# Performance work log

Measured on AMD Instinct MI355X. Metric: run time of the kernel, lower is better.

Reference implementation:

```python
import jax, jax.numpy as jnp
import numpy as np

B, N, C = 64, 256, 1024
H = 16
D = C // H            # head_dim = 64
HALF = D // 2         # rope dim per axis = 32
PT = 16               # hw_seq_len
THETA = 10000.0


def build_rope_tables():
    # VisionRotaryEmbeddingFast: per-axis freqs, repeated r=2, 2D broadcat
    freqs = 1.0 / (THETA ** (np.arange(0, HALF, 2, dtype=np.float32) / HALF))  # [HALF/2]=16
    t = np.arange(PT, dtype=np.float32)                                        # ft==pt -> t=arange
    f = t[:, None] * freqs[None, :]                                            # [16,16]
    f = np.repeat(f, 2, axis=-1)                                               # [16,32]
    f2d = np.concatenate(
        [np.broadcast_to(f[:, None, :], (PT, PT, HALF)),
         np.broadcast_to(f[None, :, :], (PT, PT, HALF))], axis=-1)             # [16,16,64]
    f2d = f2d.reshape(PT * PT, D)                                              # [256,64]
    return jnp.asarray(np.cos(f2d)), jnp.asarray(np.sin(f2d))


def rotate_half(t):
    # (..., d) -> pairwise (x0,x1) -> (-x1, x0)
    t2 = t.reshape(*t.shape[:-1], -1, 2)
    return jnp.stack([-t2[..., 1], t2[..., 0]], axis=-1).reshape(t.shape)


def apply_rope(t, cos, sin):
    # t: [B,H,N,D]; cos/sin: [N,D]
    return t * cos + rotate_half(t) * sin


def setup_inputs() -> dict:
    key = jax.random.key(0)
    k1, k2, k3 = jax.random.split(key, 3)
    x = jax.random.normal(k1, (B, N, C), dtype=jnp.float32)
    mask = jnp.ones((1, 1, N, N), dtype=bool)  # True = attend (SDPA bool mask)
    qkv_w = jax.random.normal(k2, (3 * C, C), dtype=jnp.float32) * 0.02
    qkv_b = jnp.zeros((3 * C,), dtype=jnp.float32)
    proj_w = jax.random.normal(k3, (C, C), dtype=jnp.float32) * 0.02
    proj_b = jnp.zeros((C,), dtype=jnp.float32)
    rope_cos, rope_sin = build_rope_tables()
    return {"x": x, "mask": mask, "qkv_w": qkv_w, "qkv_b": qkv_b,
            "proj_w": proj_w, "proj_b": proj_b,
            "rope_cos": rope_cos, "rope_sin": rope_sin}


def reference(x, mask, qkv_w, qkv_b, proj_w, proj_b, rope_cos, rope_sin):
    b, n, c = x.shape
    scale = 1.0 / jnp.sqrt(jnp.asarray(D, x.dtype))
    qkv = x @ qkv_w.T + qkv_b                              # [B,N,3C]
    qkv = qkv.reshape(b, n, 3, H, D).transpose(2, 0, 3, 1, 4)  # [3,B,H,N,D]
    q, k, v = qkv[0], qkv[1], qkv[2]
    q = apply_rope(q, rope_cos, rope_sin)
    k = apply_rope(k, rope_cos, rope_sin)
    scores = jnp.einsum('bhnd,bhmd->bhnm', q, k) * scale   # [B,H,N,N]
    neg = jnp.asarray(jnp.finfo(scores.dtype).min, scores.dtype)
    scores = jnp.where(mask, scores, neg)
    attn = jax.nn.softmax(scores, axis=-1)
    out = jnp.einsum('bhnm,bhmd->bhnd', attn, v)           # [B,H,N,D]
    out = out.transpose(0, 2, 1, 3).reshape(b, n, c)       # [B,N,C]
    return out @ proj_w.T + proj_b
```

## Files before the change

### kernel.cpp

```cpp
#include <hip/hip_runtime.h>
#include <math.h>

typedef short s16x8 __attribute__((ext_vector_type(8)));
typedef float f32x4 __attribute__((ext_vector_type(4)));

#define DEV static __device__ __forceinline__

DEV unsigned short f2bf(float f){
  unsigned int u = __builtin_bit_cast(unsigned int, f);
  u += 0x7fffu + ((u >> 16) & 1u);
  return (unsigned short)(u >> 16);
}

DEV void gload_lds16(const void* g, void* l){
  __builtin_amdgcn_global_load_lds(
      (const __attribute__((address_space(1))) unsigned int*)g,
      (__attribute__((address_space(3))) unsigned int*)l,
      16, 0, 0);
}

__global__ void cvt_bf16(const float* __restrict__ in, short* __restrict__ out, int n8){
  int i = blockIdx.x*blockDim.x + threadIdx.x;
  if (i >= n8) return;
  const float* p = in + (size_t)i*8;
  f32x4 a = *(const f32x4*)(p);
  f32x4 b = *(const f32x4*)(p+4);
  s16x8 o;
#pragma unroll
  for (int j=0;j<4;++j){ o[j] = (short)f2bf(a[j]); o[4+j] = (short)f2bf(b[j]); }
  *(s16x8*)(out + (size_t)i*8) = o;
}

template<int EPI>
DEV void stage_half(const short* __restrict__ Ag, const short* __restrict__ Bg,
                    char* buf, int m0, int n0, int k0, int wid, int lane, int half){
  const int l8 = lane >> 3, l7 = lane & 7;
  const int cole = ((l7 ^ l8) << 3) + k0;
#pragma unroll
  for (int j = 0; j < 2; ++j){
    const int chunk = (half*2 + j)*8 + wid;
    const short* src = Ag + (size_t)(m0 + chunk*8 + l8)*1024 + cole;
    gload_lds16(src, buf + chunk*1024);
  }
  {
    const int chunk = half*8 + wid;
    const short* src = Bg + (size_t)(n0 + chunk*8 + l8)*1024 + cole;
    gload_lds16(src, buf + 32768 + chunk*1024);
  }
}

template<int EPI>
__global__ __launch_bounds__(512, 2)
void gemm_dp(const short* __restrict__ A, const short* __restrict__ Bw,
             const float* __restrict__ bias,
             const float* __restrict__ cosT, const float* __restrict__ sinT,
             short* __restrict__ q_out, short* __restrict__ k_out, short* __restrict__ v_out,
             float* __restrict__ f_out)
{
  constexpr int K  = 1024;
  constexpr int BK = 64;
  constexpr int NT = K / BK;
  constexpr int NX = (EPI == 0) ? 24 : 8;
  constexpr int TB = 49152;
  __shared__ char smem[3 * TB];

  const int tid  = threadIdx.x;
  const int lane = tid & 63;
  const int wid  = tid >> 6;
  const int wm   = wid >> 2;
  const int wn   = wid & 3;
  const int lr   = lane & 15;
  const int lk   = lane >> 4;

  const int nwg = NX * 64;
  const int bid = blockIdx.x;
  const int cpx = nwg >> 3;
  const int swz = (bid & 7) * cpx + (bid >> 3);
  const int mt  = swz / NX;
  int nt        = swz % NX;
  if (mt & 1) nt = NX - 1 - nt;
  const int m0  = mt * 256;
  const int n0  = nt * 128;

  char* b0 = smem;
  char* b1 = smem + TB;
  char* b2 = smem + 2*TB;

  stage_half<EPI>(A, Bw, b0, m0, n0, 0,  wid, lane, 0);
  stage_half<EPI>(A, Bw, b0, m0, n0, 0,  wid, lane, 1);
  stage_half<EPI>(A, Bw, b1, m0, n0, BK, wid, lane, 0);
  stage_half<EPI>(A, Bw, b1, m0, n0, BK, wid, lane, 1);
  asm volatile("s_waitcnt vmcnt(6)" ::: "memory");
  asm volatile("s_barrier" ::: "memory");

  f32x4 acc[8][2] = {};

  for (int t = 0; t < NT; ++t){
    const int ks = (t + 2 < NT ? (t + 2) : (NT - 1)) * BK;
#pragma unroll
    for (int kk = 0; kk < 2; ++kk){
      s16x8 af[8], bf[2];
      const int cb = kk*64 + lk*16;
#pragma unroll
      for (int m = 0; m < 8; ++m){
        const int row = wm*128 + m*16 + lr;
        af[m] = *(const s16x8*)(b0 + row*128 + (cb ^ ((row & 7) << 4)));
      }
#pragma unroll
      for (int n = 0; n < 2; ++n){
        const int row = wn*32 + n*16 + lr;
        bf[n] = *(const s16x8*)(b0 + 32768 + row*128 + (cb ^ ((row & 7) << 4)));
      }
      stage_half<EPI>(A, Bw, b2, m0, n0, ks, wid, lane, kk);
      asm volatile("s_barrier" ::: "memory");
      __builtin_amdgcn_s_setprio(1);
#pragma unroll
      for (int m = 0; m < 8; ++m)
#pragma unroll
        for (int n = 0; n < 2; ++n)
          acc[m][n] = __builtin_amdgcn_mfma_f32_16x16x32_bf16(af[m], bf[n], acc[m][n], 0, 0, 0);
      __builtin_amdgcn_s_setprio(0);
    }
    asm volatile("s_waitcnt vmcnt(6)" ::: "memory");
    asm volatile("s_barrier" ::: "memory");
    char* tmp = b0; b0 = b1; b1 = b2; b2 = tmp;
  }
  asm volatile("s_waitcnt vmcnt(0)" ::: "memory");

  if constexpr (EPI == 0){
    const int sel = n0 >> 10;
    short* dst0 = (sel == 0) ? q_out : k_out;
#pragma unroll
    for (int m = 0; m < 8; ++m){
#pragma unroll
      for (int n = 0; n < 2; ++n){
        const int col  = n0 + wn*32 + n*16 + lr;
        const int rowb = m0 + wm*128 + m*16 + lk*4;
        const float bv = bias[col];
        const int rem = col & 1023;
        const int h = rem >> 6, d = rem & 63;
        if (sel < 2){
#pragma unroll
          for (int r = 0; r < 4; ++r){
            const int row = rowb + r;
            const int ntok = row & 255, b = row >> 8;
            float v = acc[m][n][r] + bv;
            float partner = __shfl_xor(v, 1, 64);
            float rot = (lane & 1) ? partner : -partner;
            float o = v * cosT[ntok*64 + d] + rot * sinT[ntok*64 + d];
            if (sel == 0) o *= 0.125f;
            dst0[(((size_t)b*16 + h)*256 + ntok)*64 + d] = (short)f2bf(o);
          }
        } else {
          const int ntok = rowb & 255, b = rowb >> 8;
          unsigned long long pk = 0;
#pragma unroll
          for (int r = 0; r < 4; ++r)
            pk |= ((unsigned long long)f2bf(acc[m][n][r] + bv)) << (16*r);
          *(unsigned long long*)(v_out + (((size_t)b*16 + h)*64 + d)*256 + ntok) = pk;
        }
      }
    }
  } else {
#pragma unroll
    for (int m = 0; m < 8; ++m){
#pragma unroll
      for (int n = 0; n < 2; ++n){
        const int col  = n0 + wn*32 + n*16 + lr;
        const int rowb = m0 + wm*128 + m*16 + lk*4;
        const float bv = bias[col];
#pragma unroll
        for (int r = 0; r < 4; ++r)
          f_out[(size_t)(rowb + r)*1024 + col] = acc[m][n][r] + bv;
      }
    }
  }
}

__global__ __launch_bounds__(512)
void attn_kernel(const short* __restrict__ qh, const short* __restrict__ kh,
                 const short* __restrict__ vt, short* __restrict__ ao)
{
  __shared__ short Ks[256*64];
  __shared__ short Vs[64*256];
  __shared__ short Ps[8][32*64];
  const int tid  = threadIdx.x;
  const int lane = tid & 63;
  const int wid  = tid >> 6;
  const int lr   = lane & 15;
  const int lk   = lane >> 4;
  const int bh = blockIdx.x;
  const size_t base = (size_t)bh * 256 * 64;
  const short* Kg = kh + base;
  const short* Qg = qh + base;
  const short* Vg = vt + base;

#pragma unroll
  for (int p=0; p<4; ++p){
    int flat = (p*512 + tid)*8;
    uint4 kv = *(const uint4*)(Kg + flat);
    int krow = flat >> 6;  int kcb = (flat & 63)*2;
    *(uint4*)((char*)Ks + krow*128 + (kcb ^ ((krow&7)<<4))) = kv;
    uint4 vv = *(const uint4*)(Vg + flat);
    int vrow = flat >> 8;  int vcb = (flat & 255)*2;
    *(uint4*)((char*)Vs + vrow*512 + (vcb ^ ((vrow&7)<<4))) = vv;
  }

  const int qbase = wid*32;
  s16x8 qf[2][2];
#pragma unroll
  for (int qr=0; qr<2; ++qr)
#pragma unroll
    for (int ks=0; ks<2; ++ks)
      qf[qr][ks] = *(const s16x8*)(Qg + (size_t)(qbase + qr*16 + lr)*64 + ks*32 + lk*8);

  __syncthreads();

  float mrun[2][4], lrun[2][4];
  f32x4 o[2][4] = {};
#pragma unroll
  for (int qr=0; qr<2; ++qr)
#pragma unroll
    for (int r=0; r<4; ++r){ mrun[qr][r] = -INFINITY; lrun[qr][r] = 0.f; }

  for (int t=0; t<4; ++t){
    f32x4 s[2][4] = {};
#pragma unroll
    for (int kc=0; kc<4; ++kc){
      const int row = t*64 + kc*16 + lr;
#pragma unroll
      for (int ks=0; ks<2; ++ks){
        const int cb = ks*64 + lk*16;
        s16x8 kf = *(const s16x8*)((char*)Ks + row*128 + (cb ^ ((row&7)<<4)));
#pragma unroll
        for (int qr=0; qr<2; ++qr)
          s[qr][kc] = __builtin_amdgcn_mfma_f32_16x16x32_bf16(qf[qr][ks], kf, s[qr][kc], 0, 0, 0);
      }
    }
#pragma unroll
    for (int qr=0; qr<2; ++qr)
#pragma unroll
      for (int r=0; r<4; ++r){
        float mx = fmaxf(fmaxf(s[qr][0][r], s[qr][1][r]), fmaxf(s[qr][2][r], s[qr][3][r]));
        mx = fmaxf(mx, __shfl_xor(mx, 1, 64));
        mx = fmaxf(mx, __shfl_xor(mx, 2, 64));
        mx = fmaxf(mx, __shfl_xor(mx, 4, 64));
        mx = fmaxf(mx, __shfl_xor(mx, 8, 64));
        const float mnew  = fmaxf(mrun[qr][r], mx);
        const float alpha = __expf(mrun[qr][r] - mnew);
        float rsum = 0.f;
#pragma unroll
        for (int kc=0; kc<4; ++kc){
          float p = __expf(s[qr][kc][r] - mnew);
          s[qr][kc][r] = p;
          rsum += p;
        }
        rsum += __shfl_xor(rsum, 1, 64);
        rsum += __shfl_xor(rsum, 2, 64);
        rsum += __shfl_xor(rsum, 4, 64);
        rsum += __shfl_xor(rsum, 8, 64);
        lrun[qr][r] = lrun[qr][r]*alpha + rsum;
        mrun[qr][r] = mnew;
#pragma unroll
        for (int oc=0; oc<4; ++oc) o[qr][oc][r] *= alpha;
      }
#pragma unroll
    for (int qr=0; qr<2; ++qr)
#pragma unroll
      for (int kc=0; kc<4; ++kc)
#pragma unroll
        for (int r=0; r<4; ++r){
          const int row = qr*16 + lk*4 + r;
          const int cb  = (kc*16 + lr)*2;
          *(short*)((char*)&Ps[wid][0] + row*128 + (cb ^ ((row&7)<<4))) = (short)f2bf(s[qr][kc][r]);
        }
#pragma unroll
    for (int ks2=0; ks2<2; ++ks2){
      s16x8 pf[2];
#pragma unroll
      for (int qr=0; qr<2; ++qr){
        const int row = qr*16 + lr;
        const int cb  = ks2*64 + lk*16;
        pf[qr] = *(const s16x8*)((char*)&Ps[wid][0] + row*128 + (cb ^ ((row&7)<<4)));
      }
#pragma unroll
      for (int oc=0; oc<4; ++oc){
        const int vrow = oc*16 + lr;
        const int vcb  = t*128 + ks2*64 + lk*16;
        s16x8 vf = *(const s16x8*)((char*)Vs + vrow*512 + (vcb ^ ((vrow&7)<<4)));
#pragma unroll
        for (int qr=0; qr<2; ++qr)
          o[qr][oc] = __builtin_amdgcn_mfma_f32_16x16x32_bf16(pf[qr], vf, o[qr][oc], 0, 0, 0);
      }
    }
  }

  const int b = bh >> 4, h = bh & 15;
#pragma unroll
  for (int qr=0; qr<2; ++qr)
#pragma unroll
    for (int oc=0; oc<4; ++oc)
#pragma unroll
      for (int r=0; r<4; ++r){
        const int n = qbase + qr*16 + lk*4 + r;
        const int d = oc*16 + lr;
        float val = o[qr][oc][r] / lrun[qr][r];
        ao[(size_t)(b*256 + n)*1024 + h*64 + d] = (short)f2bf(val);
      }
}

extern "C" void kernel_launch(void* const* d_in, const int* in_sizes, int n_in,
                              void* d_out, int out_size, void* d_ws, size_t ws_size,
                              hipStream_t stream)
{
  const float* x      = (const float*)d_in[0];
  const float* qkv_w  = (const float*)d_in[2];
  const float* qkv_b  = (const float*)d_in[3];
  const float* proj_w = (const float*)d_in[4];
  const float* proj_b = (const float*)d_in[5];
  const float* rc     = (const float*)d_in[6];
  const float* rs     = (const float*)d_in[7];

  char* ws = (char*)d_ws;
  short* xbf   = (short*)(ws);
  short* wqkv  = (short*)(ws + 33554432);
  short* wproj = (short*)(ws + 39845888);
  short* qhb   = (short*)(ws + 41943040);
  short* khb   = (short*)(ws + 75497472);
  short* vtb   = (short*)(ws + 109051904);
  short* aob   = xbf;

  cvt_bf16<<<8192, 256, 0, stream>>>(x,      xbf,   2097152);
  cvt_bf16<<<1536, 256, 0, stream>>>(qkv_w,  wqkv,   393216);
  cvt_bf16<<< 512, 256, 0, stream>>>(proj_w, wproj,  131072);

  gemm_dp<0><<<1536, 512, 0, stream>>>(xbf, wqkv, qkv_b, rc, rs,
                                       qhb, khb, vtb, nullptr);
  attn_kernel<<<1024, 512, 0, stream>>>(qhb, khb, vtb, aob);
  gemm_dp<1><<<512, 512, 0, stream>>>(aob, wproj, proj_b, nullptr, nullptr,
                                      nullptr, nullptr, nullptr, (float*)d_out);
}
```

Before: 386.9 us.

## Enlarge GEMM tiles to 256x256, double-buffer LDS, fuse bf16 conversions into one launch

The GEMM tile grows from 256x128 to 256x256, with each wave computing 8x4 MFMA blocks, which raises arithmetic intensity per staged byte. The triple-buffered half-stage pipeline with mid-iteration barriers becomes a simpler double buffer that waits for all loads at the end of each k-step. The three fp32-to-bf16 conversion launches merge into one kernel that picks its source by index range. In exchange, accumulator registers double (risking spills under launch_bounds(512,2)), LDS use is 128KB, grids shrink to 768 and 256 blocks, which may underfill the 256 CUs, and less load latency is hidden.

```diff
diff --git a/kernel.cpp b/kernel.cpp
--- a/kernel.cpp
+++ b/kernel.cpp
@@ -19,50 +19,54 @@
       16, 0, 0);
 }
 
-__global__ void cvt_bf16(const float* __restrict__ in, short* __restrict__ out, int n8){
+__global__ void cvt_all(const float* __restrict__ x,  const float* __restrict__ w1,
+                        const float* __restrict__ w2,
+                        short* __restrict__ ox, short* __restrict__ o1,
+                        short* __restrict__ o2){
   int i = blockIdx.x*blockDim.x + threadIdx.x;
-  if (i >= n8) return;
-  const float* p = in + (size_t)i*8;
+  const float* src; short* dst; int j;
+  if (i < 2097152)      { src = x;  dst = ox; j = i; }
+  else if (i < 2490368) { src = w1; dst = o1; j = i - 2097152; }
+  else                  { src = w2; dst = o2; j = i - 2490368; }
+  const float* p = src + (size_t)j*8;
   f32x4 a = *(const f32x4*)(p);
   f32x4 b = *(const f32x4*)(p+4);
   s16x8 o;
 #pragma unroll
-  for (int j=0;j<4;++j){ o[j] = (short)f2bf(a[j]); o[4+j] = (short)f2bf(b[j]); }
-  *(s16x8*)(out + (size_t)i*8) = o;
-}
-
-template<int EPI>
-DEV void stage_half(const short* __restrict__ Ag, const short* __restrict__ Bg,
-                    char* buf, int m0, int n0, int k0, int wid, int lane, int half){
+  for (int t=0;t<4;++t){ o[t] = (short)f2bf(a[t]); o[4+t] = (short)f2bf(b[t]); }
+  *(s16x8*)(dst + (size_t)j*8) = o;
+}
+
+DEV void stage_tile(const short* __restrict__ Ag, const short* __restrict__ Bg,
+                    char* buf, int m0, int n0, int k0, int wid, int lane){
   const int l8 = lane >> 3, l7 = lane & 7;
   const int cole = ((l7 ^ l8) << 3) + k0;
 #pragma unroll
-  for (int j = 0; j < 2; ++j){
-    const int chunk = (half*2 + j)*8 + wid;
-    const short* src = Ag + (size_t)(m0 + chunk*8 + l8)*1024 + cole;
-    gload_lds16(src, buf + chunk*1024);
-  }
-  {
-    const int chunk = half*8 + wid;
-    const short* src = Bg + (size_t)(n0 + chunk*8 + l8)*1024 + cole;
-    gload_lds16(src, buf + 32768 + chunk*1024);
+  for (int j = 0; j < 4; ++j){
+    const int c = j*8 + wid;
+    const short* src = Ag + (size_t)(m0 + c*8 + l8)*1024 + cole;
+    gload_lds16(src, buf + c*1024);
+  }
+#pragma unroll
+  for (int j = 0; j < 4; ++j){
+    const int c = j*8 + wid;
+    const short* src = Bg + (size_t)(n0 + c*8 + l8)*1024 + cole;
+    gload_lds16(src, buf + 32768 + c*1024);
   }
 }
 
 template<int EPI>
 __global__ __launch_bounds__(512, 2)
-void gemm_dp(const short* __restrict__ A, const short* __restrict__ Bw,
+void gemm_v3(const short* __restrict__ A, const short* __restrict__ Bw,
              const float* __restrict__ bias,
              const float* __restrict__ cosT, const float* __restrict__ sinT,
              short* __restrict__ q_out, short* __restrict__ k_out, short* __restrict__ v_out,
              float* __restrict__ f_out)
 {
-  constexpr int K  = 1024;
   constexpr int BK = 64;
-  constexpr int NT = K / BK;
-  constexpr int NX = (EPI == 0) ? 24 : 8;
-  constexpr int TB = 49152;
-  __shared__ char smem[3 * TB];
+  constexpr int NT = 1024 / BK;
+  constexpr int NX = (EPI == 0) ? 12 : 4;
+  __shared__ char smem[2 * 65536];
 
   const int tid  = threadIdx.x;
   const int lane = tid & 63;
@@ -80,52 +84,44 @@
   int nt        = swz % NX;
   if (mt & 1) nt = NX - 1 - nt;
   const int m0  = mt * 256;
-  const int n0  = nt * 128;
-
-  char* b0 = smem;
-  char* b1 = smem + TB;
-  char* b2 = smem + 2*TB;
-
-  stage_half<EPI>(A, Bw, b0, m0, n0, 0,  wid, lane, 0);
-  stage_half<EPI>(A, Bw, b0, m0, n0, 0,  wid, lane, 1);
-  stage_half<EPI>(A, Bw, b1, m0, n0, BK, wid, lane, 0);
-  stage_half<EPI>(A, Bw, b1, m0, n0, BK, wid, lane, 1);
-  asm volatile("s_waitcnt vmcnt(6)" ::: "memory");
+  const int n0  = nt * 256;
+
+  stage_tile(A, Bw, smem, m0, n0, 0, wid, lane);
+  asm volatile("s_waitcnt vmcnt(0)" ::: "memory");
   asm volatile("s_barrier" ::: "memory");
 
-  f32x4 acc[8][2] = {};
+  f32x4 acc[8][4] = {};
 
   for (int t = 0; t < NT; ++t){
-    const int ks = (t + 2 < NT ? (t + 2) : (NT - 1)) * BK;
+    char* rb = smem + (t & 1) * 65536;
+    char* sb = smem + ((t + 1) & 1) * 65536;
+    if (t + 1 < NT)
+      stage_tile(A, Bw, sb, m0, n0, (t + 1) * BK, wid, lane);
 #pragma unroll
     for (int kk = 0; kk < 2; ++kk){
-      s16x8 af[8], bf[2];
+      s16x8 af[8], bf[4];
       const int cb = kk*64 + lk*16;
 #pragma unroll
       for (int m = 0; m < 8; ++m){
         const int row = wm*128 + m*16 + lr;
-        af[m] = *(const s16x8*)(b0 + row*128 + (cb ^ ((row & 7) << 4)));
-      }
-#pragma unroll
-      for (int n = 0; n < 2; ++n){
-        const int row = wn*32 + n*16 + lr;
-        bf[n] = *(const s16x8*)(b0 + 32768 + row*128 + (cb ^ ((row & 7) << 4)));
-      }
-      stage_half<EPI>(A, Bw, b2, m0, n0, ks, wid, lane, kk);
-      asm volatile("s_barrier" ::: "memory");
+        af[m] = *(const s16x8*)(rb + row*128 + (cb ^ ((row & 7) << 4)));
+      }
+#pragma unroll
+      for (int n = 0; n < 4; ++n){
+        const int row = wn*64 + n*16 + lr;
+        bf[n] = *(const s16x8*)(rb + 32768 + row*128 + (cb ^ ((row & 7) << 4)));
+      }
       __builtin_amdgcn_s_setprio(1);
 #pragma unroll
       for (int m = 0; m < 8; ++m)
 #pragma unroll
-        for (int n = 0; n < 2; ++n)
+        for (int n = 0; n < 4; ++n)
           acc[m][n] = __builtin_amdgcn_mfma_f32_16x16x32_bf16(af[m], bf[n], acc[m][n], 0, 0, 0);
       __builtin_amdgcn_s_setprio(0);
     }
-    asm volatile("s_waitcnt vmcnt(6)" ::: "memory");
+    asm volatile("s_waitcnt vmcnt(0)" ::: "memory");
     asm volatile("s_barrier" ::: "memory");
-    char* tmp = b0; b0 = b1; b1 = b2; b2 = tmp;
-  }
-  asm volatile("s_waitcnt vmcnt(0)" ::: "memory");
+  }
 
   if constexpr (EPI == 0){
     const int sel = n0 >> 10;
@@ -133,8 +129,8 @@
 #pragma unroll
     for (int m = 0; m < 8; ++m){
 #pragma unroll
-      for (int n = 0; n < 2; ++n){
-        const int col  = n0 + wn*32 + n*16 + lr;
+      for (int n = 0; n < 4; ++n){
+        const int col  = n0 + wn*64 + n*16 + lr;
         const int rowb = m0 + wm*128 + m*16 + lk*4;
         const float bv = bias[col];
         const int rem = col & 1023;
@@ -165,8 +161,8 @@
 #pragma unroll
     for (int m = 0; m < 8; ++m){
 #pragma unroll
-      for (int n = 0; n < 2; ++n){
-        const int col  = n0 + wn*32 + n*16 + lr;
+      for (int n = 0; n < 4; ++n){
+        const int col  = n0 + wn*64 + n*16 + lr;
         const int rowb = m0 + wm*128 + m*16 + lk*4;
         const float bv = bias[col];
 #pragma unroll
@@ -330,13 +326,11 @@
   short* vtb   = (short*)(ws + 109051904);
   short* aob   = xbf;
 
-  cvt_bf16<<<8192, 256, 0, stream>>>(x,      xbf,   2097152);
-  cvt_bf16<<<1536, 256, 0, stream>>>(qkv_w,  wqkv,   393216);
-  cvt_bf16<<< 512, 256, 0, stream>>>(proj_w, wproj,  131072);
-
-  gemm_dp<0><<<1536, 512, 0, stream>>>(xbf, wqkv, qkv_b, rc, rs,
-                                       qhb, khb, vtb, nullptr);
+  cvt_all<<<10240, 256, 0, stream>>>(x, qkv_w, proj_w, xbf, wqkv, wproj);
+
+  gemm_v3<0><<<768, 512, 0, stream>>>(xbf, wqkv, qkv_b, rc, rs,
+                                      qhb, khb, vtb, nullptr);
   attn_kernel<<<1024, 512, 0, stream>>>(qhb, khb, vtb, aob);
-  gemm_dp<1><<<512, 512, 0, stream>>>(aob, wproj, proj_b, nullptr, nullptr,
+  gemm_v3<1><<<256, 512, 0, stream>>>(aob, wproj, proj_b, nullptr, nullptr,
                                       nullptr, nullptr, nullptr, (float*)d_out);
 }
```

Measured after the change: 358.7 us. 1.08x faster.
